# Optimization experiments

Hardware: AMD Instinct MI355X
Metric: run time of the kernel (lower is better)

Reference implementation:

```python
import jax, jax.numpy as jnp
import numpy as np
import math

B, S, HID = 4, 2048, 1024
N_HEADS, HEAD_DIM = 16, 64
LOGITS_CAP = 30.0
EPS = 1e-6

def setup_inputs() -> dict:
    key = jax.random.key(0)
    ks = jax.random.split(key, 8)
    sd = 1.0 / math.sqrt(HID)
    return {
        "hidden_states": jax.random.normal(ks[0], (B, S, HID), dtype=jnp.float32),
        "attention_mask": jnp.zeros((B, 1, 1, S), dtype=jnp.float32),
        "Wq": jax.random.normal(ks[1], (HID, HID), dtype=jnp.float32) * sd,
        "bq": jnp.zeros((HID,), dtype=jnp.float32),
        "Wk": jax.random.normal(ks[2], (HID, HID), dtype=jnp.float32) * sd,
        "bk": jnp.zeros((HID,), dtype=jnp.float32),
        "Wv": jax.random.normal(ks[3], (HID, HID), dtype=jnp.float32) * sd,
        "bv": jnp.zeros((HID,), dtype=jnp.float32),
    }

def _heads(x):
    # [B,S,HID] -> [B,N_HEADS,S,HEAD_DIM]
    return x.reshape(B, S, N_HEADS, HEAD_DIM).transpose(0, 2, 1, 3)

def reference(hidden_states, attention_mask, Wq, bq, Wk, bk, Wv, bv):
    # QKV projections (torch Linear: x @ W.T + b)
    q = _heads(jnp.einsum('bsh,oh->bso', hidden_states, Wq) + bq)
    k = _heads(jnp.einsum('bsh,oh->bso', hidden_states, Wk) + bk)
    v = _heads(jnp.einsum('bsh,oh->bso', hidden_states, Wv) + bv)
    # raw scores [B,H,S,S], scaled (softmax_2RELU path uses 1/sqrt(d))
    scores = jnp.einsum('bnqd,bnkd->bnqk', q, k) / math.sqrt(HEAD_DIM)
    scores = scores + attention_mask
    # tanh logit soft-capping
    scores = jnp.tanh(scores / LOGITS_CAP) * LOGITS_CAP
    # softmax_2RELU: relu(x) / (sum relu(x) + eps)
    r = jax.nn.relu(scores)
    probs = r / (jnp.sum(r, axis=-1, keepdims=True) + EPS)
    # context [B,H,S,D] -> [B,S,HID]
    ctx = jnp.einsum('bnqk,bnkd->bnqd', probs, v)
    return ctx.transpose(0, 2, 1, 3).reshape(B, S, HID)
```

## Files before the change

kernel.cpp:

```cpp
#include <hip/hip_runtime.h>
#include <hip/hip_bf16.h>

#define B_    4
#define S_    2048
#define HID_  1024
#define NH_   16
#define HD_   64
#define C3_  (-3.7037037037e-4f)
#define C5_  (1.64609053498e-7f)

typedef __attribute__((ext_vector_type(8))) short short8;
typedef __attribute__((ext_vector_type(4))) float float4v;

static __device__ __forceinline__ unsigned short f2bf(float f) {
    unsigned u = __builtin_bit_cast(unsigned, f);
    u = (u + 0x7fffu + ((u >> 16) & 1u)) >> 16;
    return (unsigned short)u;
}

__global__ void convert_all(const float* __restrict__ h,
                            const float* __restrict__ wq,
                            const float* __restrict__ wk,
                            const float* __restrict__ wv,
                            unsigned short* __restrict__ hb,
                            unsigned short* __restrict__ wqb,
                            unsigned short* __restrict__ wkb,
                            unsigned short* __restrict__ wvb) {
    const int which = blockIdx.y;
    const float* src = (which == 0) ? h : (which == 1) ? wq : (which == 2) ? wk : wv;
    unsigned short* dst = (which == 0) ? hb : (which == 1) ? wqb : (which == 2) ? wkb : wvb;
    const float sc = (which == 1) ? 0.125f : 1.0f;
    const int n4 = ((which == 0) ? (B_ * S_ * HID_) : (HID_ * HID_)) / 4;
    int i = blockIdx.x * blockDim.x + threadIdx.x;
    const int st = gridDim.x * blockDim.x;
    for (; i < n4; i += st) {
        float4 v = ((const float4*)src)[i];
        ushort4 o;
        o.x = f2bf(v.x * sc); o.y = f2bf(v.y * sc); o.z = f2bf(v.z * sc); o.w = f2bf(v.w * sc);
        ((ushort4*)dst)[i] = o;
    }
}

__global__ __launch_bounds__(256) void qkv_gemm(
    const unsigned short* __restrict__ hb,
    const unsigned short* __restrict__ wqb,
    const unsigned short* __restrict__ wkb,
    const unsigned short* __restrict__ wvb,
    const float* __restrict__ bq,
    const float* __restrict__ bk,
    const float* __restrict__ bv,
    unsigned short* __restrict__ q_ws,
    unsigned short* __restrict__ k_ws,
    unsigned short* __restrict__ vt_ws) {
    const int z = blockIdx.z;
    const unsigned short* wgt = (z == 0) ? wqb : ((z == 1) ? wkb : wvb);
    const float* bias = (z == 0) ? bq : ((z == 1) ? bk : bv);
    const bool zswap = (z == 2);
    const int arow0 = zswap ? blockIdx.x * 128 : blockIdx.y * 128;
    const int brow0 = zswap ? blockIdx.y * 128 : blockIdx.x * 128;
    const unsigned short* At = zswap ? wgt : hb;
    const unsigned short* Bt = zswap ? hb : wgt;

    __shared__ unsigned short As[128 * 64];
    __shared__ unsigned short Bs[128 * 64];

    const int tid = threadIdx.x;
    const int lane = tid & 63;
    const int w = tid >> 6;
    const int wm = w >> 1, wn = w & 1;
    const int l15 = lane & 15;
    const int g = lane >> 4;

    const int srow = lane >> 3;
    const int schunk = (lane & 7) ^ srow;
    const int scol = schunk * 8;

    const int xm = (l15 & 7) << 4;
    const int roff0 = l15 * 128 + ((g * 16) ^ xm);
    const int roff1 = l15 * 128 + ((g * 16 + 64) ^ xm);

    float4v acc[4][4] = {};

    for (int k0 = 0; k0 < HID_; k0 += 64) {
#pragma unroll
        for (int j = 0; j < 4; j++) {
            const int row = j * 32 + w * 8 + srow;
            const unsigned short* gA = &At[(size_t)(arow0 + row) * HID_ + k0 + scol];
            const unsigned short* gB = &Bt[(size_t)(brow0 + row) * HID_ + k0 + scol];
            __builtin_amdgcn_global_load_lds(
                (const __attribute__((address_space(1))) unsigned int*)gA,
                (__attribute__((address_space(3))) unsigned int*)((char*)As + (j * 32 + w * 8) * 128),
                16, 0, 0);
            __builtin_amdgcn_global_load_lds(
                (const __attribute__((address_space(1))) unsigned int*)gB,
                (__attribute__((address_space(3))) unsigned int*)((char*)Bs + (j * 32 + w * 8) * 128),
                16, 0, 0);
        }
        __syncthreads();

        short8 af0[4], af1[4], bf0[4], bf1[4];
#pragma unroll
        for (int mf = 0; mf < 4; mf++) {
            const char* ab = (const char*)As + (wm * 64 + mf * 16) * 128;
            af0[mf] = *(const short8*)(ab + roff0);
            af1[mf] = *(const short8*)(ab + roff1);
        }
#pragma unroll
        for (int nf = 0; nf < 4; nf++) {
            const char* bb = (const char*)Bs + (wn * 64 + nf * 16) * 128;
            bf0[nf] = *(const short8*)(bb + roff0);
            bf1[nf] = *(const short8*)(bb + roff1);
        }
#pragma unroll
        for (int mf = 0; mf < 4; mf++)
#pragma unroll
            for (int nf = 0; nf < 4; nf++) {
                acc[mf][nf] = __builtin_amdgcn_mfma_f32_16x16x32_bf16(af0[mf], bf0[nf], acc[mf][nf], 0, 0, 0);
                acc[mf][nf] = __builtin_amdgcn_mfma_f32_16x16x32_bf16(af1[mf], bf1[nf], acc[mf][nf], 0, 0, 0);
            }
        __syncthreads();
    }

    if (!zswap) {
#pragma unroll
        for (int mf = 0; mf < 4; mf++)
#pragma unroll
            for (int nf = 0; nf < 4; nf++) {
                const int o = brow0 + wn * 64 + nf * 16 + l15;
                const float bb = bias[o] * ((z == 0) ? 0.125f : 1.0f);
                const int h = o >> 6, d = o & 63;
#pragma unroll
                for (int r = 0; r < 4; r++) {
                    const int m = arow0 + wm * 64 + mf * 16 + g * 4 + r;
                    const int b = m >> 11, s = m & 2047;
                    const unsigned short bfv = f2bf(acc[mf][nf][r] + bb);
                    if (z == 0)
                        q_ws[(((size_t)(b * NH_ + h)) * S_ + s) * HD_ + d] = bfv;
                    else
                        k_ws[(((size_t)(b * NH_ + h)) * S_ + s) * HD_ + d] = bfv;
                }
            }
    } else {
#pragma unroll
        for (int mf = 0; mf < 4; mf++) {
            const int obase = arow0 + wm * 64 + mf * 16 + g * 4;
            float bbr[4];
#pragma unroll
            for (int r = 0; r < 4; r++) bbr[r] = bias[obase + r];
#pragma unroll
            for (int nf = 0; nf < 4; nf++) {
                const int m = brow0 + wn * 64 + nf * 16 + l15;
                const int b = m >> 11, s = m & 2047;
#pragma unroll
                for (int r = 0; r < 4; r++) {
                    const int o = obase + r;
                    const int h = o >> 6, d = o & 63;
                    vt_ws[(((size_t)(b * NH_ + h)) * HD_ + d) * S_ + s] =
                        f2bf(acc[mf][nf][r] + bbr[r]);
                }
            }
        }
    }
}

__global__ __launch_bounds__(512, 4) void attn_kernel(
    const unsigned short* __restrict__ q_ws,
    const unsigned short* __restrict__ k_ws,
    const unsigned short* __restrict__ vt_ws,
    const float* __restrict__ mask,
    float* __restrict__ out) {
    const int id = blockIdx.y * 8 + blockIdx.x;
    const int x = id & 7, i = id >> 3;
    const int bh = x * 8 + (i >> 3);
    const int qt = i & 7;
    const int b = bh >> 4, h = bh & 15;
    const unsigned short* qp = q_ws + (size_t)bh * S_ * HD_;
    const unsigned short* kp = k_ws + (size_t)bh * S_ * HD_;
    const unsigned short* vp = vt_ws + (size_t)bh * HD_ * S_;
    const float* mp = mask + (size_t)b * S_;

    __shared__ unsigned short Kl[2][64 * 64];
    __shared__ unsigned short Vl[2][64 * 64];
    __shared__ unsigned short Pl[8][32][72];

    const int tid = threadIdx.x, lane = tid & 63, w = tid >> 6;
    const int l15 = lane & 15;
    const int g = lane >> 4;
    const int kk = g * 8;

    const int srow = lane >> 3;
    const int schunk = (lane & 7) ^ srow;
    const int scol = schunk * 8;

    const int xm = (l15 & 7) << 4;
    const int roff0 = l15 * 128 + ((g * 16) ^ xm);
    const int roff1 = l15 * 128 + ((g * 16 + 64) ^ xm);

    short8 qf[2][2];
#pragma unroll
    for (int t = 0; t < 2; t++) {
        const int qrow = qt * 256 + w * 32 + t * 16 + l15;
        qf[t][0] = *(const short8*)&qp[(size_t)qrow * HD_ + kk];
        qf[t][1] = *(const short8*)&qp[(size_t)qrow * HD_ + 32 + kk];
    }

    const short8 ones = {0x3F80, 0x3F80, 0x3F80, 0x3F80, 0x3F80, 0x3F80, 0x3F80, 0x3F80};

    float4v ctx[2][4] = {};
    float4v ctxS[2] = {};

    auto stage = [&](int kt, int buf) {
        const unsigned short* gK =
            &kp[(size_t)(kt * 64 + w * 8 + srow) * HD_ + scol];
        __builtin_amdgcn_global_load_lds(
            (const __attribute__((address_space(1))) unsigned int*)gK,
            (__attribute__((address_space(3))) unsigned int*)((char*)&Kl[buf][0] + (w * 8) * 128),
            16, 0, 0);
        const unsigned short* gV =
            &vp[(size_t)(w * 8 + srow) * S_ + kt * 64 + scol];
        __builtin_amdgcn_global_load_lds(
            (const __attribute__((address_space(1))) unsigned int*)gV,
            (__attribute__((address_space(3))) unsigned int*)((char*)&Vl[buf][0] + (w * 8) * 128),
            16, 0, 0);
    };

    stage(0, 0);
    asm volatile("s_waitcnt vmcnt(0)" ::: "memory");
    __builtin_amdgcn_s_barrier();

    int cur = 0;
    for (int kt = 0; kt < 32; kt++) {
        if (kt < 31) stage(kt + 1, cur ^ 1);

        const char* kb = (const char*)&Kl[cur][0];
        float4v sfr[2][4];
#pragma unroll
        for (int n = 0; n < 4; n++) {
            short8 kf0 = *(const short8*)(kb + n * 2048 + roff0);
            short8 kf1 = *(const short8*)(kb + n * 2048 + roff1);
#pragma unroll
            for (int t = 0; t < 2; t++) {
                float4v a = {};
                a = __builtin_amdgcn_mfma_f32_16x16x32_bf16(kf0, qf[t][0], a, 0, 0, 0);
                a = __builtin_amdgcn_mfma_f32_16x16x32_bf16(kf1, qf[t][1], a, 0, 0, 0);
                sfr[t][n] = a;
            }
        }

#pragma unroll
        for (int n = 0; n < 4; n++) {
            const float4 mq = *(const float4*)&mp[kt * 64 + n * 16 + g * 4];
            const float mr[4] = {mq.x, mq.y, mq.z, mq.w};
#pragma unroll
            for (int t = 0; t < 2; t++) {
                float rl[4];
#pragma unroll
                for (int r = 0; r < 4; r++) {
                    float s = sfr[t][n][r] + mr[r];
                    float u = s * s;
                    float su = s * u;
                    float tt = __builtin_fmaf(u, C5_, C3_);
                    float p = __builtin_fmaf(su, tt, s);
                    rl[r] = fmaxf(p, 0.0f);
                }
                unsigned int d01, d23;
                asm("v_cvt_pk_bf16_f32 %0, %1, %2" : "=v"(d01) : "v"(rl[0]), "v"(rl[1]));
                asm("v_cvt_pk_bf16_f32 %0, %1, %2" : "=v"(d23) : "v"(rl[2]), "v"(rl[3]));
                uint2 pv;
                pv.x = d01; pv.y = d23;
                *(uint2*)&Pl[w][t * 16 + l15][n * 16 + g * 4] = pv;
            }
        }

        short8 pf[2][2];
#pragma unroll
        for (int t = 0; t < 2; t++) {
            pf[t][0] = *(const short8*)&Pl[w][t * 16 + l15][kk];
            pf[t][1] = *(const short8*)&Pl[w][t * 16 + l15][32 + kk];
            ctxS[t] = __builtin_amdgcn_mfma_f32_16x16x32_bf16(pf[t][0], ones, ctxS[t], 0, 0, 0);
            ctxS[t] = __builtin_amdgcn_mfma_f32_16x16x32_bf16(pf[t][1], ones, ctxS[t], 0, 0, 0);
        }
        const char* vb = (const char*)&Vl[cur][0];
#pragma unroll
        for (int n = 0; n < 4; n++) {
            short8 vf0 = *(const short8*)(vb + n * 2048 + roff0);
            short8 vf1 = *(const short8*)(vb + n * 2048 + roff1);
#pragma unroll
            for (int t = 0; t < 2; t++) {
                ctx[t][n] = __builtin_amdgcn_mfma_f32_16x16x32_bf16(pf[t][0], vf0, ctx[t][n], 0, 0, 0);
                ctx[t][n] = __builtin_amdgcn_mfma_f32_16x16x32_bf16(pf[t][1], vf1, ctx[t][n], 0, 0, 0);
            }
        }

        asm volatile("s_waitcnt vmcnt(0)" ::: "memory");
        __builtin_amdgcn_s_barrier();
        cur ^= 1;
    }

#pragma unroll
    for (int t = 0; t < 2; t++) {
        float rinv[4];
#pragma unroll
        for (int r = 0; r < 4; r++)
            rinv[r] = __builtin_amdgcn_rcpf(ctxS[t][r] + 1e-6f);
#pragma unroll
        for (int n = 0; n < 4; n++) {
            const int d = n * 16 + l15;
#pragma unroll
            for (int r = 0; r < 4; r++) {
                const int qrow = qt * 256 + w * 32 + t * 16 + g * 4 + r;
                out[((size_t)b * S_ + qrow) * HID_ + h * HD_ + d] = ctx[t][n][r] * rinv[r];
            }
        }
    }
}

extern "C" void kernel_launch(void* const* d_in, const int* in_sizes, int n_in,
                              void* d_out, int out_size, void* d_ws, size_t ws_size,
                              hipStream_t stream) {
    const float* hidden = (const float*)d_in[0];
    const float* mask   = (const float*)d_in[1];
    const float* Wq     = (const float*)d_in[2];
    const float* bq     = (const float*)d_in[3];
    const float* Wk     = (const float*)d_in[4];
    const float* bk     = (const float*)d_in[5];
    const float* Wv     = (const float*)d_in[6];
    const float* bv     = (const float*)d_in[7];
    float* out = (float*)d_out;

    char* ws = (char*)d_ws;
    const size_t HB_BYTES = (size_t)B_ * S_ * HID_ * 2;
    const size_t W_BYTES  = (size_t)HID_ * HID_ * 2;
    const size_t QKV_BYTES = (size_t)B_ * NH_ * S_ * HD_ * 2;

    unsigned short* hb    = (unsigned short*)(ws);
    unsigned short* wqb   = (unsigned short*)(ws + HB_BYTES);
    unsigned short* wkb   = (unsigned short*)(ws + HB_BYTES + W_BYTES);
    unsigned short* wvb   = (unsigned short*)(ws + HB_BYTES + 2 * W_BYTES);
    unsigned short* q_wsp = (unsigned short*)(ws + HB_BYTES + 3 * W_BYTES);
    unsigned short* k_wsp = (unsigned short*)(ws + HB_BYTES + 3 * W_BYTES + QKV_BYTES);
    unsigned short* vt_wsp = (unsigned short*)(ws + HB_BYTES + 3 * W_BYTES + 2 * QKV_BYTES);

    dim3 cgrid(1024, 4);
    convert_all<<<cgrid, 256, 0, stream>>>(hidden, Wq, Wk, Wv, hb, wqb, wkb, wvb);

    dim3 ggrid(HID_ / 128, (B_ * S_) / 128, 3);
    qkv_gemm<<<ggrid, 256, 0, stream>>>(hb, wqb, wkb, wvb, bq, bk, bv,
                                        q_wsp, k_wsp, vt_wsp);

    dim3 agrid(S_ / 256, B_ * NH_);
    attn_kernel<<<agrid, 512, 0, stream>>>(q_wsp, k_wsp, vt_wsp, mask, out);
}
```

Baseline: 265.2 us.

## Keep P in registers via permuted K staging and coalesce output stores

The K tile is staged with permuted key rows so that the score MFMA output layout already matches the B-operand layout of the P·V MFMA. The probabilities therefore stay in registers and the per-warp LDS round trip through Pl goes away. The MFMA operand order is swapped to match, and the mask load index is permuted to follow. The epilogue now transposes output through shared scratch so each thread writes float4 rows instead of scattered scalar stores, at the cost of extra barriers and reuse of the K/V shared buffer.

```diff
diff --git a/kernel.cpp b/kernel.cpp
--- a/kernel.cpp
+++ b/kernel.cpp
@@ -11,6 +11,7 @@
 
 typedef __attribute__((ext_vector_type(8))) short short8;
 typedef __attribute__((ext_vector_type(4))) float float4v;
+typedef __attribute__((ext_vector_type(4))) unsigned int uint4v;
 
 static __device__ __forceinline__ unsigned short f2bf(float f) {
     unsigned u = __builtin_bit_cast(unsigned, f);
@@ -179,9 +180,7 @@
     const unsigned short* vp = vt_ws + (size_t)bh * HD_ * S_;
     const float* mp = mask + (size_t)b * S_;
 
-    __shared__ unsigned short Kl[2][64 * 64];
-    __shared__ unsigned short Vl[2][64 * 64];
-    __shared__ unsigned short Pl[8][32][72];
+    __shared__ __align__(16) char smem[34816];
 
     const int tid = threadIdx.x, lane = tid & 63, w = tid >> 6;
     const int l15 = lane & 15;
@@ -192,6 +191,10 @@
     const int schunk = (lane & 7) ^ srow;
     const int scol = schunk * 8;
 
+    const int rho = w * 8 + srow;
+    const int rho5 = rho & 31;
+    const int keyoff = (rho >> 5) * 32 + (((rho5 >> 2) & 3) << 3) + ((rho5 >> 4) << 2) + (rho5 & 3);
+
     const int xm = (l15 & 7) << 4;
     const int roff0 = l15 * 128 + ((g * 16) ^ xm);
     const int roff1 = l15 * 128 + ((g * 16 + 64) ^ xm);
@@ -211,16 +214,16 @@
 
     auto stage = [&](int kt, int buf) {
         const unsigned short* gK =
-            &kp[(size_t)(kt * 64 + w * 8 + srow) * HD_ + scol];
+            &kp[(size_t)(kt * 64 + keyoff) * HD_ + scol];
         __builtin_amdgcn_global_load_lds(
             (const __attribute__((address_space(1))) unsigned int*)gK,
-            (__attribute__((address_space(3))) unsigned int*)((char*)&Kl[buf][0] + (w * 8) * 128),
+            (__attribute__((address_space(3))) unsigned int*)(smem + buf * 8192 + (w * 8) * 128),
             16, 0, 0);
         const unsigned short* gV =
             &vp[(size_t)(w * 8 + srow) * S_ + kt * 64 + scol];
         __builtin_amdgcn_global_load_lds(
             (const __attribute__((address_space(1))) unsigned int*)gV,
-            (__attribute__((address_space(3))) unsigned int*)((char*)&Vl[buf][0] + (w * 8) * 128),
+            (__attribute__((address_space(3))) unsigned int*)(smem + 16384 + buf * 8192 + (w * 8) * 128),
             16, 0, 0);
     };
 
@@ -232,7 +235,7 @@
     for (int kt = 0; kt < 32; kt++) {
         if (kt < 31) stage(kt + 1, cur ^ 1);
 
-        const char* kb = (const char*)&Kl[cur][0];
+        const char* kb = smem + cur * 8192;
         float4v sfr[2][4];
 #pragma unroll
         for (int n = 0; n < 4; n++) {
@@ -247,12 +250,14 @@
             }
         }
 
-#pragma unroll
-        for (int n = 0; n < 4; n++) {
-            const float4 mq = *(const float4*)&mp[kt * 64 + n * 16 + g * 4];
-            const float mr[4] = {mq.x, mq.y, mq.z, mq.w};
-#pragma unroll
-            for (int t = 0; t < 2; t++) {
+        short8 pbf[2][2];
+#pragma unroll
+        for (int t = 0; t < 2; t++) {
+            uint4v pk[2];
+#pragma unroll
+            for (int n = 0; n < 4; n++) {
+                const float4 mq = *(const float4*)&mp[kt * 64 + (n >> 1) * 32 + g * 8 + (n & 1) * 4];
+                const float mr[4] = {mq.x, mq.y, mq.z, mq.w};
                 float rl[4];
 #pragma unroll
                 for (int r = 0; r < 4; r++) {
@@ -266,29 +271,27 @@
                 unsigned int d01, d23;
                 asm("v_cvt_pk_bf16_f32 %0, %1, %2" : "=v"(d01) : "v"(rl[0]), "v"(rl[1]));
                 asm("v_cvt_pk_bf16_f32 %0, %1, %2" : "=v"(d23) : "v"(rl[2]), "v"(rl[3]));
-                uint2 pv;
-                pv.x = d01; pv.y = d23;
-                *(uint2*)&Pl[w][t * 16 + l15][n * 16 + g * 4] = pv;
-            }
-        }
-
-        short8 pf[2][2];
+                pk[n >> 1][(n & 1) * 2]     = d01;
+                pk[n >> 1][(n & 1) * 2 + 1] = d23;
+            }
+            pbf[t][0] = __builtin_bit_cast(short8, pk[0]);
+            pbf[t][1] = __builtin_bit_cast(short8, pk[1]);
+        }
+
 #pragma unroll
         for (int t = 0; t < 2; t++) {
-            pf[t][0] = *(const short8*)&Pl[w][t * 16 + l15][kk];
-            pf[t][1] = *(const short8*)&Pl[w][t * 16 + l15][32 + kk];
-            ctxS[t] = __builtin_amdgcn_mfma_f32_16x16x32_bf16(pf[t][0], ones, ctxS[t], 0, 0, 0);
-            ctxS[t] = __builtin_amdgcn_mfma_f32_16x16x32_bf16(pf[t][1], ones, ctxS[t], 0, 0, 0);
-        }
-        const char* vb = (const char*)&Vl[cur][0];
+            ctxS[t] = __builtin_amdgcn_mfma_f32_16x16x32_bf16(ones, pbf[t][0], ctxS[t], 0, 0, 0);
+            ctxS[t] = __builtin_amdgcn_mfma_f32_16x16x32_bf16(ones, pbf[t][1], ctxS[t], 0, 0, 0);
+        }
+        const char* vb = smem + 16384 + cur * 8192;
 #pragma unroll
         for (int n = 0; n < 4; n++) {
             short8 vf0 = *(const short8*)(vb + n * 2048 + roff0);
             short8 vf1 = *(const short8*)(vb + n * 2048 + roff1);
 #pragma unroll
             for (int t = 0; t < 2; t++) {
-                ctx[t][n] = __builtin_amdgcn_mfma_f32_16x16x32_bf16(pf[t][0], vf0, ctx[t][n], 0, 0, 0);
-                ctx[t][n] = __builtin_amdgcn_mfma_f32_16x16x32_bf16(pf[t][1], vf1, ctx[t][n], 0, 0, 0);
+                ctx[t][n] = __builtin_amdgcn_mfma_f32_16x16x32_bf16(vf0, pbf[t][0], ctx[t][n], 0, 0, 0);
+                ctx[t][n] = __builtin_amdgcn_mfma_f32_16x16x32_bf16(vf1, pbf[t][1], ctx[t][n], 0, 0, 0);
             }
         }
 
@@ -297,21 +300,28 @@
         cur ^= 1;
     }
 
+    float* scr = (float*)smem;
 #pragma unroll
     for (int t = 0; t < 2; t++) {
-        float rinv[4];
-#pragma unroll
-        for (int r = 0; r < 4; r++)
-            rinv[r] = __builtin_amdgcn_rcpf(ctxS[t][r] + 1e-6f);
+        const float rinv = __builtin_amdgcn_rcpf(ctxS[t][0] + 1e-6f);
 #pragma unroll
         for (int n = 0; n < 4; n++) {
-            const int d = n * 16 + l15;
-#pragma unroll
-            for (int r = 0; r < 4; r++) {
-                const int qrow = qt * 256 + w * 32 + t * 16 + g * 4 + r;
-                out[((size_t)b * S_ + qrow) * HID_ + h * HD_ + d] = ctx[t][n][r] * rinv[r];
-            }
-        }
+            float4 v;
+            v.x = ctx[t][n][0] * rinv;
+            v.y = ctx[t][n][1] * rinv;
+            v.z = ctx[t][n][2] * rinv;
+            v.w = ctx[t][n][3] * rinv;
+            *(float4*)&scr[(w * 16 + l15) * 68 + n * 16 + g * 4] = v;
+        }
+        __builtin_amdgcn_s_barrier();
+        const int qq = lane >> 2, c = lane & 3;
+        const size_t obase = ((size_t)b * S_ + qt * 256 + w * 32 + t * 16 + qq) * HID_ + h * HD_;
+#pragma unroll
+        for (int j = 0; j < 4; j++) {
+            float4 v = *(const float4*)&scr[(w * 16 + qq) * 68 + c * 4 + j * 16];
+            *(float4*)&out[obase + c * 4 + j * 16] = v;
+        }
+        __builtin_amdgcn_s_barrier();
     }
 }
 
```

Result: faster. 257.1 us (-3.1%).
